# Optimization experiments

Hardware: AMD Instinct MI355X
Metric: run time of the kernel (lower is better)

The kernel has to match this reference:

```python
import jax, jax.numpy as jnp
import numpy as np

DEPTH, DIM, M_DIM, K = 3, 16, 16, 8  # depth, emb_dim, EGNN m_dim default, num_nearest_neighbors
LN_EPS = 1e-5


def _gather(x, idx):
    # x: [B,L,...], idx: [B,L,K] -> [B,L,K,...] (per-batch neighbor gather)
    return jax.vmap(lambda xb, ib: xb[ib])(x, idx)


def _lin(k, fi, fo):
    k1, k2 = jax.random.split(k)
    lim = 1.0 / np.sqrt(fi)
    w = jax.random.uniform(k1, (fi, fo), minval=-lim, maxval=lim, dtype=jnp.float32)
    b = jax.random.uniform(k2, (fo,), minval=-lim, maxval=lim, dtype=jnp.float32)
    return w, b


def _stacked(k, fi, fo):
    ws, bs = zip(*[_lin(kk, fi, fo) for kk in jax.random.split(k, DEPTH)])
    return jnp.stack(ws), jnp.stack(bs)


def setup_inputs() -> dict:
    key = jax.random.key(0)
    ks = jax.random.split(key, 16)
    B, L, num_tokens = 16, 1024, 2
    edge_in = 2 * DIM + 1  # feats_i, feats_j, rel_dist
    inp = {}
    inp['coords'] = jax.random.normal(ks[0], (B, L, 3), dtype=jnp.float32) * 3.0
    inp['residues'] = jax.random.randint(ks[1], (B, L), 0, num_tokens)
    inp['lengths'] = jax.random.randint(ks[2], (B,), L // 2, L + 1)
    inp['token_emb'] = jax.random.normal(ks[3], (num_tokens, DIM), dtype=jnp.float32)
    inp['pos_emb'] = jax.random.normal(ks[4], (L, DIM), dtype=jnp.float32)
    inp['edge_w1'], inp['edge_b1'] = _stacked(ks[5], edge_in, edge_in * 2)
    inp['edge_w2'], inp['edge_b2'] = _stacked(ks[6], edge_in * 2, M_DIM)
    inp['coors_w1'], inp['coors_b1'] = _stacked(ks[7], M_DIM, M_DIM * 4)
    inp['coors_w2'], inp['coors_b2'] = _stacked(ks[8], M_DIM * 4, 1)
    inp['ln_g'] = jnp.ones((DEPTH, DIM), jnp.float32)
    inp['ln_b'] = jnp.zeros((DEPTH, DIM), jnp.float32)
    inp['node_w1'], inp['node_b1'] = _stacked(ks[9], DIM + M_DIM, DIM * 2)
    inp['node_w2'], inp['node_b2'] = _stacked(ks[10], DIM * 2, DIM)
    inp['final_w'], inp['final_b'] = _lin(ks[11], DIM, 3)
    return inp


def reference(coords, residues, lengths, token_emb, pos_emb,
              edge_w1, edge_b1, edge_w2, edge_b2,
              coors_w1, coors_b1, coors_w2, coors_b2,
              ln_g, ln_b, node_w1, node_b1, node_w2, node_b2,
              final_w, final_b):
    B, L, _ = coords.shape
    silu = jax.nn.silu
    mask = jnp.arange(L)[None, :] < lengths[:, None]                 # [B,L]
    pair_mask = mask[:, :, None] & mask[:, None, :]                  # [B,L,L]
    eye = jnp.eye(L, dtype=bool)
    # chain adjacency: i <-> i+1 where both endpoints are within length
    r = jnp.arange(L - 1)
    chain = jnp.zeros((L, L), bool).at[r, r + 1].set(True)
    chain = chain | chain.T
    adj = (chain[None] & pair_mask) & ~eye                           # [B,L,L]

    feats = token_emb[residues] + pos_emb[None, :L]                  # [B,L,D]
    coors = coords
    for d in range(DEPTH):
        # pairwise squared distances for kNN ranking (memory-bound)
        rel_dist_full = jnp.sum((coors[:, :, None] - coors[:, None, :]) ** 2, -1)  # [B,L,L]
        ranking = jnp.where(pair_mask, rel_dist_full, 1e5)
        ranking = jnp.where(eye, -1.0, ranking)   # self always selected first
        ranking = jnp.where(adj, 0.0, ranking)    # adjacency edges forced in
        _, idx = jax.lax.top_k(-ranking, K)                           # [B,L,K] smallest
        mask_j = _gather(mask, idx)
        emask = mask[:, :, None] & mask_j                             # [B,L,K] (valid_radius=inf)
        coors_j = _gather(coors, idx)                                 # [B,L,K,3]
        rel_coors = coors[:, :, None] - coors_j                       # [B,L,K,3]
        rel_dist = jnp.sum(rel_coors ** 2, -1, keepdims=True)         # [B,L,K,1]
        feats_j = _gather(feats, idx)                                 # [B,L,K,D]
        feats_i = jnp.broadcast_to(feats[:, :, None], feats_j.shape)
        edge_in = jnp.concatenate([feats_i, feats_j, rel_dist], -1)   # [B,L,K,2D+1]
        h = silu(edge_in @ edge_w1[d] + edge_b1[d])
        m_ij = silu(h @ edge_w2[d] + edge_b2[d])                      # [B,L,K,M]
        # equivariant coordinate update
        w = silu(m_ij @ coors_w1[d] + coors_b1[d]) @ coors_w2[d] + coors_b2[d]
        w = jnp.where(emask[..., None], w, 0.0)[..., 0]               # [B,L,K]
        coors = coors + jnp.einsum('blk,blkc->blc', w, rel_coors)
        # node update (norm_feats=True in EGNN_Network -> LayerNorm)
        m_i = jnp.sum(jnp.where(emask[..., None], m_ij, 0.0), 2)      # [B,L,M]
        mu = feats.mean(-1, keepdims=True)
        var = jnp.mean((feats - mu) ** 2, -1, keepdims=True)
        normed = (feats - mu) / jnp.sqrt(var + LN_EPS) * ln_g[d] + ln_b[d]
        nin = jnp.concatenate([normed, m_i], -1)                      # [B,L,D+M]
        feats = feats + (silu(nin @ node_w1[d] + node_b1[d]) @ node_w2[d] + node_b2[d])
    delta = feats @ final_w + final_b                                 # [B,L,3]
    return delta
```

## Files before the change

### kernel.cpp

```cpp
#include <hip/hip_runtime.h>
#include <math.h>

typedef unsigned long long u64;
typedef unsigned int u32;

#define NB 16
#define SL 1024
#define DIM 16
#define MDIM 16
#define KNN 8
#define CH 64
#define NHID 32
#define LN_EPS 1e-5f
#define PST 144

__device__ __forceinline__ float silu_f(float x) {
    const float e = __expf(-x);
    return x * __builtin_amdgcn_rcpf(1.0f + e);
}

__global__ __launch_bounds__(256) void init_kernel(
    const float* __restrict__ coords, const int* __restrict__ residues,
    const float* __restrict__ token_emb, const float* __restrict__ pos_emb,
    const float* __restrict__ w1tp, const float* __restrict__ g_eb1,
    float* __restrict__ coordsA, float* __restrict__ featsA,
    float* __restrict__ Pout)
{
    const int t = blockIdx.x * 256 + threadIdx.x;
    const int node = t >> 2;
    const int part = t & 3;
    const int l = node & (SL - 1);
    const int r = residues[node];
    float f[16];
    {
        const float4* te = (const float4*)(token_emb + (size_t)r * DIM);
        const float4* pe = (const float4*)(pos_emb + (size_t)l * DIM);
#pragma unroll
        for (int q = 0; q < 4; ++q) {
            float4 a = te[q], b4 = pe[q];
            f[4*q+0] = a.x + b4.x; f[4*q+1] = a.y + b4.y;
            f[4*q+2] = a.z + b4.z; f[4*q+3] = a.w + b4.w;
        }
    }
    if (part == 0) {
        float4* fo = (float4*)(featsA + (size_t)node * DIM);
#pragma unroll
        for (int q = 0; q < 4; ++q)
            fo[q] = make_float4(f[4*q], f[4*q+1], f[4*q+2], f[4*q+3]);
        coordsA[node * 3 + 0] = coords[node * 3 + 0];
        coordsA[node * 3 + 1] = coords[node * 3 + 1];
        coordsA[node * 3 + 2] = coords[node * 3 + 2];
    }
    const int ubase = (part & 1) * 33;
    const int wbase = (part < 2) ? 0 : 66;
    float res[36];
    res[33] = 0.f; res[34] = 0.f; res[35] = 0.f;
#pragma unroll
    for (int oo = 0; oo < 33; ++oo) {
        const int u = ubase + oo;
        const float* wr = w1tp + (wbase + u) * 16;
        float a0 = (part < 2) ? g_eb1[u] : 0.0f;
        float a1 = 0.f, a2 = 0.f, a3 = 0.f;
#pragma unroll
        for (int c = 0; c < 16; c += 4) {
            a0 = fmaf(f[c + 0], wr[c + 0], a0);
            a1 = fmaf(f[c + 1], wr[c + 1], a1);
            a2 = fmaf(f[c + 2], wr[c + 2], a2);
            a3 = fmaf(f[c + 3], wr[c + 3], a3);
        }
        res[oo] = (a0 + a1) + (a2 + a3);
    }
    float4* op = (float4*)(Pout + (size_t)node * PST + part * 36);
#pragma unroll
    for (int q = 0; q < 9; ++q)
        op[q] = make_float4(res[4*q], res[4*q+1], res[4*q+2], res[4*q+3]);
}

__global__ __launch_bounds__(256) void pack_kernel(
    const float* __restrict__ ew1, const float* __restrict__ ew2,
    const float* __restrict__ cw1,
    const float* __restrict__ nw1, const float* __restrict__ nw2,
    float* __restrict__ w1tp, float* __restrict__ w1rp, float* __restrict__ w2p,
    float* __restrict__ cw1t, float* __restrict__ nw1t, float* __restrict__ nw2t)
{
    const int stride = gridDim.x * 256;
    const int t0 = blockIdx.x * 256 + threadIdx.x;
    for (int idx = t0; idx < 3 * 132 * 16; idx += stride) {
        int d = idx / (132 * 16); int r = idx - d * 132 * 16; int o = r >> 4; int c = r & 15;
        int u = (o < 66) ? o : (o - 66);
        int cc = (o < 66) ? c : (16 + c);
        w1tp[idx] = ew1[(d * 33 + cc) * 66 + u];
    }
    for (int idx = t0; idx < 3 * 72; idx += stride) {
        int d = idx / 72; int o = idx - d * 72; int hh = o / 36; int uu = o - hh * 36;
        w1rp[idx] = (uu < 33) ? ew1[(d * 33 + 32) * 66 + hh * 33 + uu] : 0.0f;
    }
    for (int idx = t0; idx < 3 * 72 * 16; idx += stride) {
        int d = idx / (72 * 16); int r = idx - d * 72 * 16; int u = r >> 4; int v = r & 15;
        int hh = u / 36; int uu = u - hh * 36;
        w2p[idx] = (uu < 33) ? ew2[(d * 66 + hh * 33 + uu) * 16 + v] : 0.0f;
    }
    for (int idx = t0; idx < 3 * CH * 16; idx += stride) {
        int d = idx / (CH * 16); int r = idx - d * CH * 16; int t = r >> 4; int v = r & 15;
        cw1t[(d * CH + t) * 16 + v] = cw1[(d * 16 + v) * CH + t];
    }
    for (int idx = t0; idx < 3 * NHID * 32; idx += stride) {
        int d = idx / (NHID * 32); int r = idx - d * NHID * 32; int u = r >> 5; int c = r & 31;
        nw1t[(d * NHID + u) * 32 + c] = nw1[(d * 32 + c) * NHID + u];
    }
    for (int idx = t0; idx < 3 * 16 * 32; idx += stride) {
        int d = idx / (16 * 32); int r = idx - d * 16 * 32; int c = r >> 5; int u = r & 31;
        nw2t[(d * 16 + c) * 32 + u] = nw2[(d * 32 + u) * 16 + c];
    }
}

__device__ __forceinline__ void merge8(u32* a, const u32* bb) {
    u32 c[8];
#pragma unroll
    for (int t = 0; t < 8; ++t) c[t] = min(a[t], bb[7 - t]);
#define MCAS(x, y) { u32 mn = min(c[x], c[y]); u32 mx = max(c[x], c[y]); c[x] = mn; c[y] = mx; }
    MCAS(0, 4) MCAS(1, 5) MCAS(2, 6) MCAS(3, 7)
    MCAS(0, 2) MCAS(1, 3) MCAS(4, 6) MCAS(5, 7)
    MCAS(0, 1) MCAS(2, 3) MCAS(4, 5) MCAS(6, 7)
#undef MCAS
#pragma unroll
    for (int t = 0; t < 8; ++t) a[t] = c[t];
}

__global__ __launch_bounds__(1024, 8) void knn_kernel(
    const float* __restrict__ coords, const int* __restrict__ lengths,
    int* __restrict__ idxbuf)
{
    __shared__ __align__(16) float4 s_cand[SL];
    __shared__ u32 lists[32][32][9];
    const int tid = threadIdx.x;
    const int b = blockIdx.x >> 5;
    const int i0 = (blockIdx.x & 31) << 5;
    const int len = lengths[b];
    const float* cb = coords + (size_t)b * SL * 3;
    for (int idx = tid; idx < SL; idx += 1024) {
        const float* cp = cb + idx * 3;
        s_cand[idx] = make_float4(cp[0], cp[1], cp[2], 0.0f);
    }
    __syncthreads();

    const int wv = tid >> 6;
    const int lane = tid & 63;
    const int q = lane & 31;
    const int s = (wv << 1) | (lane >> 5);
    const int i = i0 + q;
    const bool mi = i < len;
    const float4 qi = s_cand[i];
    const float xi = qi.x, yi = qi.y, zi = qi.z;

    u32 lst[8];
#pragma unroll
    for (int t = 0; t < 8; ++t) lst[t] = 0xFFFFFFFFu;

    const int jbase = s << 5;
#pragma unroll 4
    for (int jj = 0; jj < 32; ++jj) {
        const int j = jbase + jj;
        const float4 cj = s_cand[j];
        const float dx = xi - cj.x, dy = yi - cj.y, dz = zi - cj.z;
        const float dist = dx * dx + dy * dy + dz * dz;
        const int dij = j - i;
        const bool pm = mi && (j < len);
        const bool adjx = (dij == 1) | (dij == -1);
        float v = pm ? (adjx ? 0.0f : dist) : 1e5f;
        v = (dij == 0) ? -1.0f : v;
        u32 bits = __float_as_uint(v);
        bits ^= (u32)((int)bits >> 31) | 0x80000000u;
        const u32 key = (bits & 0xFFFFFC00u) | (u32)j;
#pragma unroll
        for (int p = 7; p >= 1; --p)
            lst[p] = min(max(key, lst[p - 1]), lst[p]);
        lst[0] = min(key, lst[0]);
    }

#pragma unroll
    for (int t = 0; t < 8; ++t) lists[s][q][t] = lst[t];
    __syncthreads();

    if (tid < 512) {
        const int p = tid >> 5, qq = tid & 31;
        u32 a[8], bb[8];
#pragma unroll
        for (int t = 0; t < 8; ++t) { a[t] = lists[2 * p][qq][t]; bb[t] = lists[2 * p + 1][qq][t]; }
        merge8(a, bb);
#pragma unroll
        for (int t = 0; t < 8; ++t) lists[2 * p][qq][t] = a[t];
    }
    __syncthreads();
    if (tid < 256) {
        const int p = tid >> 5, qq = tid & 31;
        u32 a[8], bb[8];
#pragma unroll
        for (int t = 0; t < 8; ++t) { a[t] = lists[4 * p][qq][t]; bb[t] = lists[4 * p + 2][qq][t]; }
        merge8(a, bb);
#pragma unroll
        for (int t = 0; t < 8; ++t) lists[4 * p][qq][t] = a[t];
    }
    __syncthreads();
    if (tid < 128) {
        const int p = tid >> 5, qq = tid & 31;
        u32 a[8], bb[8];
#pragma unroll
        for (int t = 0; t < 8; ++t) { a[t] = lists[8 * p][qq][t]; bb[t] = lists[8 * p + 4][qq][t]; }
        merge8(a, bb);
#pragma unroll
        for (int t = 0; t < 8; ++t) lists[8 * p][qq][t] = a[t];
    }
    __syncthreads();
    if (tid < 64) {
        const int p = tid >> 5, qq = tid & 31;
        u32 a[8], bb[8];
#pragma unroll
        for (int t = 0; t < 8; ++t) { a[t] = lists[16 * p][qq][t]; bb[t] = lists[16 * p + 8][qq][t]; }
        merge8(a, bb);
#pragma unroll
        for (int t = 0; t < 8; ++t) lists[16 * p][qq][t] = a[t];
    }
    __syncthreads();
    if (tid < 32) {
        const int qq = tid;
        u32 a[8], bb[8];
#pragma unroll
        for (int t = 0; t < 8; ++t) { a[t] = lists[0][qq][t]; bb[t] = lists[16][qq][t]; }
        merge8(a, bb);
        const size_t node = (size_t)b * SL + i0 + qq;
        int4 r0 = make_int4((int)(a[0] & 1023u), (int)(a[1] & 1023u), (int)(a[2] & 1023u), (int)(a[3] & 1023u));
        int4 r1 = make_int4((int)(a[4] & 1023u), (int)(a[5] & 1023u), (int)(a[6] & 1023u), (int)(a[7] & 1023u));
        ((int4*)idxbuf)[node * 2 + 0] = r0;
        ((int4*)idxbuf)[node * 2 + 1] = r1;
    }
}

__global__ __launch_bounds__(256, 3) void layer_kernel(
    const int d,
    const float* __restrict__ coordsIn, float* __restrict__ coordsOut,
    const float* __restrict__ featsIn, float* __restrict__ featsOut,
    const float* __restrict__ Pbuf,
    const int* __restrict__ idxbuf, const int* __restrict__ lengths,
    const float* __restrict__ w1rp, const float* __restrict__ w2p,
    const float* __restrict__ g_eb2,
    const float* __restrict__ cw1t, const float* __restrict__ g_cb1,
    const float* __restrict__ g_cw2, const float* __restrict__ g_cb2,
    const float* __restrict__ g_lng, const float* __restrict__ g_lnb,
    const float* __restrict__ nw1t, const float* __restrict__ g_nb1,
    const float* __restrict__ nw2t, const float* __restrict__ g_nb2,
    const float* __restrict__ w1tp_all, const float* __restrict__ g_eb1,
    float* __restrict__ PbufOut)
{
    __shared__ float s_w2e[72 * 16];
    __shared__ __align__(16) float s_w1r[72];
    __shared__ float s_cw1[CH * 16];
    __shared__ float s_cw2v[CH];
    __shared__ float s_nw1[NHID * 36];
    __shared__ float s_nw2[16 * 36];
    __shared__ float s_eb2[16], s_cb1[CH];
    __shared__ float s_lng[16], s_lnb[16], s_nb1[32], s_nb2[16];
    __shared__ float s_cb2v;

    const int tid = threadIdx.x;
    for (int t = tid; t < 72 * 16; t += 256) s_w2e[t] = w2p[d * 72 * 16 + t];
    for (int t = tid; t < CH * 16; t += 256) s_cw1[t] = cw1t[d * CH * 16 + t];
    for (int t = tid; t < NHID * 32; t += 256) s_nw1[(t >> 5) * 36 + (t & 31)] = nw1t[d * NHID * 32 + t];
    for (int t = tid; t < 16 * 32; t += 256) s_nw2[(t >> 5) * 36 + (t & 31)] = nw2t[d * 16 * 32 + t];
    if (tid < 72) s_w1r[tid] = w1rp[d * 72 + tid];
    if (tid < CH) { s_cw2v[tid] = g_cw2[d * CH + tid]; s_cb1[tid] = g_cb1[d * CH + tid]; }
    if (tid < 16) {
        s_eb2[tid] = g_eb2[d * 16 + tid];
        s_lng[tid] = g_lng[d * 16 + tid];
        s_lnb[tid] = g_lnb[d * 16 + tid];
        s_nb2[tid] = g_nb2[d * 16 + tid];
    }
    if (tid < 32) s_nb1[tid] = g_nb1[d * 32 + tid];
    if (tid == 0) s_cb2v = g_cb2[d];

    const int lane = tid & 63;
    const int h = (lane >> 3) & 1;
    const int k = lane & 7;
    const int sub = lane & 15;
    const int nA = blockIdx.x * 32 + (tid >> 4);
    const int nB = nA + 16;
    const int b = nA >> 10;
    const int len = lengths[b];
    const int jA = idxbuf[nA * 8 + k];
    const int jB = idxbuf[nB * 8 + k];
    const bool emA = ((nA & 1023) < len) && (jA < len);
    const bool emB = ((nB & 1023) < len) && (jB < len);

    float ciA[3], relA[3], ciB[3], relB[3];
    {
        const float* cpA = coordsIn + (size_t)nA * 3;
        const float* cqA = coordsIn + ((size_t)b * SL + jA) * 3;
        ciA[0] = cpA[0]; ciA[1] = cpA[1]; ciA[2] = cpA[2];
        relA[0] = ciA[0] - cqA[0]; relA[1] = ciA[1] - cqA[1]; relA[2] = ciA[2] - cqA[2];
        const float* cpB = coordsIn + (size_t)nB * 3;
        const float* cqB = coordsIn + ((size_t)b * SL + jB) * 3;
        ciB[0] = cpB[0]; ciB[1] = cpB[1]; ciB[2] = cpB[2];
        relB[0] = ciB[0] - cqB[0]; relB[1] = ciB[1] - cqB[1]; relB[2] = ciB[2] - cqB[2];
    }
    const float rdA = fmaf(relA[0], relA[0], fmaf(relA[1], relA[1], relA[2] * relA[2]));
    const float rdB = fmaf(relB[0], relB[0], fmaf(relB[1], relB[1], relB[2] * relB[2]));

    const int ub = h * 36;
    const float* PiA = Pbuf + (size_t)nA * PST + ub;
    const float* PjA = Pbuf + ((size_t)b * SL + jA) * PST + 72 + ub;
    const float* PiB = Pbuf + (size_t)nB * PST + ub;
    const float* PjB = Pbuf + ((size_t)b * SL + jB) * PST + 72 + ub;

    __syncthreads();

    float maccA[16], maccB[16];
#pragma unroll
    for (int v = 0; v < 16; ++v) {
        const float e0 = h ? 0.0f : s_eb2[v];
        maccA[v] = e0; maccB[v] = e0;
    }
#pragma unroll
    for (int c4 = 0; c4 < 9; ++c4) {
        const float4 paA = *(const float4*)(PiA + 4 * c4);
        const float4 pbA = *(const float4*)(PjA + 4 * c4);
        const float4 paB = *(const float4*)(PiB + 4 * c4);
        const float4 pbB = *(const float4*)(PjB + 4 * c4);
        const int u0 = ub + c4 * 4;
        const float4 w1r4 = *(const float4*)&s_w1r[u0];
        const float huA0 = silu_f(fmaf(rdA, w1r4.x, paA.x + pbA.x));
        const float huA1 = silu_f(fmaf(rdA, w1r4.y, paA.y + pbA.y));
        const float huA2 = silu_f(fmaf(rdA, w1r4.z, paA.z + pbA.z));
        const float huA3 = silu_f(fmaf(rdA, w1r4.w, paA.w + pbA.w));
        const float huB0 = silu_f(fmaf(rdB, w1r4.x, paB.x + pbB.x));
        const float huB1 = silu_f(fmaf(rdB, w1r4.y, paB.y + pbB.y));
        const float huB2 = silu_f(fmaf(rdB, w1r4.z, paB.z + pbB.z));
        const float huB3 = silu_f(fmaf(rdB, w1r4.w, paB.w + pbB.w));
        const float* w2r = &s_w2e[u0 * 16];
#pragma unroll
        for (int v = 0; v < 16; ++v) {
            const float w0 = w2r[v], w1 = w2r[16 + v], w2_ = w2r[32 + v], w3 = w2r[48 + v];
            maccA[v] = fmaf(huA3, w3, fmaf(huA2, w2_, fmaf(huA1, w1, fmaf(huA0, w0, maccA[v]))));
            maccB[v] = fmaf(huB3, w3, fmaf(huB2, w2_, fmaf(huB1, w1, fmaf(huB0, w0, maccB[v]))));
        }
    }

#pragma unroll
    for (int v = 0; v < 16; ++v) {
        maccA[v] = silu_f(maccA[v] + __shfl_xor(maccA[v], 8, 64));
        maccB[v] = silu_f(maccB[v] + __shfl_xor(maccB[v], 8, 64));
    }

    const int tb = h * 32;
    float waA = 0.f, waB = 0.f;
#pragma unroll 4
    for (int tt = 0; tt < 32; ++tt) {
        const float* cr = &s_cw1[(tb + tt) * 16];
        const float bias = s_cb1[tb + tt];
        float a0A = bias, a1A = 0.f, a0B = bias, a1B = 0.f;
#pragma unroll
        for (int v = 0; v < 16; v += 2) {
            a0A = fmaf(maccA[v], cr[v], a0A);
            a1A = fmaf(maccA[v + 1], cr[v + 1], a1A);
            a0B = fmaf(maccB[v], cr[v], a0B);
            a1B = fmaf(maccB[v + 1], cr[v + 1], a1B);
        }
        const float cw2v = s_cw2v[tb + tt];
        waA = fmaf(silu_f(a0A + a1A), cw2v, waA);
        waB = fmaf(silu_f(a0B + a1B), cw2v, waB);
    }
    const float waoA = __shfl_xor(waA, 8, 64);
    const float waoB = __shfl_xor(waB, 8, 64);
    const float weA = emA ? (waA + waoA + s_cb2v) : 0.f;
    const float weB = emB ? (waB + waoB + s_cb2v) : 0.f;

    float wr0A = weA * relA[0], wr1A = weA * relA[1], wr2A = weA * relA[2];
    float wr0B = weB * relB[0], wr1B = weB * relB[1], wr2B = weB * relB[2];
#pragma unroll
    for (int s = 1; s < 8; s <<= 1) {
        wr0A += __shfl_xor(wr0A, s, 64);
        wr1A += __shfl_xor(wr1A, s, 64);
        wr2A += __shfl_xor(wr2A, s, 64);
        wr0B += __shfl_xor(wr0B, s, 64);
        wr1B += __shfl_xor(wr1B, s, 64);
        wr2B += __shfl_xor(wr2B, s, 64);
    }
    if ((lane & 15) == 0) {
        coordsOut[(size_t)nA * 3 + 0] = ciA[0] + wr0A;
        coordsOut[(size_t)nA * 3 + 1] = ciA[1] + wr1A;
        coordsOut[(size_t)nA * 3 + 2] = ciA[2] + wr2A;
        coordsOut[(size_t)nB * 3 + 0] = ciB[0] + wr0B;
        coordsOut[(size_t)nB * 3 + 1] = ciB[1] + wr1B;
        coordsOut[(size_t)nB * 3 + 2] = ciB[2] + wr2B;
    }

#pragma unroll
    for (int v = 0; v < 16; ++v) {
        maccA[v] = emA ? maccA[v] : 0.f;
        maccB[v] = emB ? maccB[v] : 0.f;
#pragma unroll
        for (int s = 1; s < 8; s <<= 1) {
            maccA[v] += __shfl_xor(maccA[v], s, 64);
            maccB[v] += __shfl_xor(maccB[v], s, 64);
        }
    }

    float fiA[16], fiB[16];
    {
        const float4* ppA = (const float4*)(featsIn + (size_t)nA * DIM);
        float4 a0 = ppA[0], a1 = ppA[1], a2 = ppA[2], a3 = ppA[3];
        fiA[0]=a0.x; fiA[1]=a0.y; fiA[2]=a0.z; fiA[3]=a0.w;
        fiA[4]=a1.x; fiA[5]=a1.y; fiA[6]=a1.z; fiA[7]=a1.w;
        fiA[8]=a2.x; fiA[9]=a2.y; fiA[10]=a2.z; fiA[11]=a2.w;
        fiA[12]=a3.x; fiA[13]=a3.y; fiA[14]=a3.z; fiA[15]=a3.w;
        const float4* ppB = (const float4*)(featsIn + (size_t)nB * DIM);
        float4 b0 = ppB[0], b1 = ppB[1], b2 = ppB[2], b3 = ppB[3];
        fiB[0]=b0.x; fiB[1]=b0.y; fiB[2]=b0.z; fiB[3]=b0.w;
        fiB[4]=b1.x; fiB[5]=b1.y; fiB[6]=b1.z; fiB[7]=b1.w;
        fiB[8]=b2.x; fiB[9]=b2.y; fiB[10]=b2.z; fiB[11]=b2.w;
        fiB[12]=b3.x; fiB[13]=b3.y; fiB[14]=b3.z; fiB[15]=b3.w;
    }
    const float fiSubA = featsIn[(size_t)nA * DIM + sub];
    const float fiSubB = featsIn[(size_t)nB * DIM + sub];

    {
        float mu = 0.f;
#pragma unroll
        for (int c = 0; c < 16; ++c) mu += fiA[c];
        mu *= 0.0625f;
        float var = 0.f;
#pragma unroll
        for (int c = 0; c < 16; ++c) { const float dd = fiA[c] - mu; var = fmaf(dd, dd, var); }
        var *= 0.0625f;
        const float rs = rsqrtf(var + LN_EPS);
#pragma unroll
        for (int c = 0; c < 16; ++c) fiA[c] = fmaf((fiA[c] - mu) * rs, s_lng[c], s_lnb[c]);
    }
    {
        float mu = 0.f;
#pragma unroll
        for (int c = 0; c < 16; ++c) mu += fiB[c];
        mu *= 0.0625f;
        float var = 0.f;
#pragma unroll
        for (int c = 0; c < 16; ++c) { const float dd = fiB[c] - mu; var = fmaf(dd, dd, var); }
        var *= 0.0625f;
        const float rs = rsqrtf(var + LN_EPS);
#pragma unroll
        for (int c = 0; c < 16; ++c) fiB[c] = fmaf((fiB[c] - mu) * rs, s_lng[c], s_lnb[c]);
    }

    float nhA[2], nhB[2];
#pragma unroll
    for (int q = 0; q < 2; ++q) {
        const int u = sub * 2 + q;
        const float* nr = &s_nw1[u * 36];
        const float bias = s_nb1[u];
        float a0A = bias, a1A = 0.f, a0B = bias, a1B = 0.f;
#pragma unroll
        for (int c = 0; c < 16; c += 2) {
            a0A = fmaf(fiA[c], nr[c], a0A);
            a1A = fmaf(fiA[c + 1], nr[c + 1], a1A);
            a0B = fmaf(fiB[c], nr[c], a0B);
            a1B = fmaf(fiB[c + 1], nr[c + 1], a1B);
        }
#pragma unroll
        for (int v = 0; v < 16; v += 2) {
            a0A = fmaf(maccA[v], nr[16 + v], a0A);
            a1A = fmaf(maccA[v + 1], nr[16 + v + 1], a1A);
            a0B = fmaf(maccB[v], nr[16 + v], a0B);
            a1B = fmaf(maccB[v + 1], nr[16 + v + 1], a1B);
        }
        nhA[q] = silu_f(a0A + a1A);
        nhB[q] = silu_f(a0B + a1B);
    }

    const int nbase = lane & ~15;
    const float* w2c = &s_nw2[sub * 36];
    float oA = s_nb2[sub], oB = s_nb2[sub];
#pragma unroll
    for (int u = 0; u < 32; ++u) {
        const float w = w2c[u];
        oA = fmaf(__shfl(nhA[u & 1], nbase + (u >> 1), 64), w, oA);
        oB = fmaf(__shfl(nhB[u & 1], nbase + (u >> 1), 64), w, oB);
    }
    const float foA = fiSubA + oA;
    const float foB = fiSubB + oB;
    featsOut[(size_t)nA * DIM + sub] = foA;
    featsOut[(size_t)nB * DIM + sub] = foB;

    if (d < 2) {
        float frA[16], frB[16];
#pragma unroll
        for (int c = 0; c < 16; ++c) {
            frA[c] = __shfl(foA, nbase + c, 64);
            frB[c] = __shfl(foB, nbase + c, 64);
        }
        const float* wbase = w1tp_all + (d + 1) * 132 * 16;
        const float* bbase = g_eb1 + (d + 1) * 66;
        float* PoutA = PbufOut + (size_t)nA * PST;
        float* PoutB = PbufOut + (size_t)nB * PST;
#pragma unroll
        for (int q = 0; q < 9; ++q) {
            const int col = sub + (q << 4);
            const int ch = (col >= 108) ? 3 : (col >= 72) ? 2 : (col >= 36) ? 1 : 0;
            const int uu = col - ch * 36;
            const bool valid = uu < 33;
            const int u = ((ch & 1) ? 33 : 0) + uu;
            const int uc = valid ? u : 0;
            const int widx = valid ? ((ch < 2) ? u : 66 + u) : 0;
            const float bias = (valid && ch < 2) ? bbase[uc] : 0.0f;
            float a0A = bias, a1A = 0.f, a2A = 0.f, a3A = 0.f;
            float a0B = bias, a1B = 0.f, a2B = 0.f, a3B = 0.f;
            const float* wr = wbase + widx * 16;
#pragma unroll
            for (int cc = 0; cc < 16; cc += 4) {
                const float w0 = wr[cc + 0], w1 = wr[cc + 1], w2_ = wr[cc + 2], w3 = wr[cc + 3];
                a0A = fmaf(frA[cc + 0], w0, a0A);
                a1A = fmaf(frA[cc + 1], w1, a1A);
                a2A = fmaf(frA[cc + 2], w2_, a2A);
                a3A = fmaf(frA[cc + 3], w3, a3A);
                a0B = fmaf(frB[cc + 0], w0, a0B);
                a1B = fmaf(frB[cc + 1], w1, a1B);
                a2B = fmaf(frB[cc + 2], w2_, a2B);
                a3B = fmaf(frB[cc + 3], w3, a3B);
            }
            PoutA[col] = valid ? ((a0A + a1A) + (a2A + a3A)) : 0.0f;
            PoutB[col] = valid ? ((a0B + a1B) + (a2B + a3B)) : 0.0f;
        }
    }
}

__global__ __launch_bounds__(256) void final_kernel(
    const float* __restrict__ feats, const float* __restrict__ fw,
    const float* __restrict__ fb, float* __restrict__ out)
{
    const int nid = blockIdx.x * 256 + threadIdx.x;
    if (nid >= NB * SL) return;
    float f[DIM];
#pragma unroll
    for (int c = 0; c < DIM; ++c) f[c] = feats[nid * DIM + c];
#pragma unroll
    for (int o = 0; o < 3; ++o) {
        float acc = fb[o];
#pragma unroll
        for (int c = 0; c < DIM; ++c) acc = fmaf(f[c], fw[c * 3 + o], acc);
        out[nid * 3 + o] = acc;
    }
}

extern "C" void kernel_launch(void* const* d_in, const int* in_sizes, int n_in,
                              void* d_out, int out_size, void* d_ws, size_t ws_size,
                              hipStream_t stream) {
    const float* coords    = (const float*)d_in[0];
    const int*   residues  = (const int*)d_in[1];
    const int*   lengths   = (const int*)d_in[2];
    const float* token_emb = (const float*)d_in[3];
    const float* pos_emb   = (const float*)d_in[4];
    const float* ew1 = (const float*)d_in[5];
    const float* eb1 = (const float*)d_in[6];
    const float* ew2 = (const float*)d_in[7];
    const float* eb2 = (const float*)d_in[8];
    const float* cw1 = (const float*)d_in[9];
    const float* cb1 = (const float*)d_in[10];
    const float* cw2 = (const float*)d_in[11];
    const float* cb2 = (const float*)d_in[12];
    const float* lng = (const float*)d_in[13];
    const float* lnb = (const float*)d_in[14];
    const float* nw1 = (const float*)d_in[15];
    const float* nb1 = (const float*)d_in[16];
    const float* nw2 = (const float*)d_in[17];
    const float* nb2 = (const float*)d_in[18];
    const float* fw  = (const float*)d_in[19];
    const float* fb  = (const float*)d_in[20];

    float* ws = (float*)d_ws;
    float* coordsA = ws;
    float* coordsB = coordsA + NB * SL * 3;
    float* featsA  = coordsB + NB * SL * 3;
    float* featsB  = featsA + NB * SL * DIM;
    int*   idxbuf  = (int*)(featsB + NB * SL * DIM);
    float* w1tp = (float*)(idxbuf + NB * SL * KNN);
    float* w1rp = w1tp + 3 * 132 * 16;
    float* w2p  = w1rp + 3 * 72;
    float* cw1t = w2p + 3 * 72 * 16;
    float* nw1t = cw1t + 3 * CH * 16;
    float* nw2t = nw1t + 3 * NHID * 32;
    float* PbufA = nw2t + 3 * 16 * 32;
    float* PbufB = PbufA + (size_t)NB * SL * PST;

    pack_kernel<<<32, 256, 0, stream>>>(ew1, ew2, cw1, nw1, nw2, w1tp, w1rp, w2p, cw1t, nw1t, nw2t);
    init_kernel<<<NB * SL * 4 / 256, 256, 0, stream>>>(coords, residues, token_emb, pos_emb,
                                                        w1tp, eb1, coordsA, featsA, PbufA);

    float* cIn = coordsA; float* cOut = coordsB;
    float* fIn = featsA;  float* fOut = featsB;
    float* pIn = PbufA;   float* pOut = PbufB;
    for (int d = 0; d < 3; ++d) {
        knn_kernel<<<NB * SL / 32, 1024, 0, stream>>>(cIn, lengths, idxbuf);
        layer_kernel<<<NB * SL * KNN / 256, 256, 0, stream>>>(d, cIn, cOut, fIn, fOut, pIn, idxbuf, lengths,
            w1rp, w2p, eb2, cw1t, cb1, cw2, cb2, lng, lnb, nw1t, nb1, nw2t, nb2,
            w1tp, eb1, pOut);
        float* t;
        t = cIn; cIn = cOut; cOut = t;
        t = fIn; fIn = fOut; fOut = t;
        t = pIn; pIn = pOut; pOut = t;
    }

    final_kernel<<<NB * SL / 256, 256, 0, stream>>>(fIn, fw, fb, (float*)d_out);
}
```

Before: 273.4 us.

## Fuse KNN search, layer update and final projection into one kernel per layer

Merges the separate KNN kernel and per-layer message-passing kernel into a single kernel whose blocks first compute neighbour lists for their 32 nodes and then process those same nodes, reusing one shared-memory buffer. The final linear projection is folded into the last layer's iteration, removing a launch. KNN now uses 256 threads per block with 128 candidates per thread, which reduces parallelism in the search phase and lowers occupancy hints.

```diff
diff --git a/kernel.cpp b/kernel.cpp
--- a/kernel.cpp
+++ b/kernel.cpp
@@ -7,7 +7,6 @@
 #define NB 16
 #define SL 1024
 #define DIM 16
-#define MDIM 16
 #define KNN 8
 #define CH 64
 #define NHID 32
@@ -127,121 +126,12 @@
     for (int t = 0; t < 8; ++t) a[t] = c[t];
 }
 
-__global__ __launch_bounds__(1024, 8) void knn_kernel(
-    const float* __restrict__ coords, const int* __restrict__ lengths,
-    int* __restrict__ idxbuf)
-{
-    __shared__ __align__(16) float4 s_cand[SL];
-    __shared__ u32 lists[32][32][9];
-    const int tid = threadIdx.x;
-    const int b = blockIdx.x >> 5;
-    const int i0 = (blockIdx.x & 31) << 5;
-    const int len = lengths[b];
-    const float* cb = coords + (size_t)b * SL * 3;
-    for (int idx = tid; idx < SL; idx += 1024) {
-        const float* cp = cb + idx * 3;
-        s_cand[idx] = make_float4(cp[0], cp[1], cp[2], 0.0f);
-    }
-    __syncthreads();
-
-    const int wv = tid >> 6;
-    const int lane = tid & 63;
-    const int q = lane & 31;
-    const int s = (wv << 1) | (lane >> 5);
-    const int i = i0 + q;
-    const bool mi = i < len;
-    const float4 qi = s_cand[i];
-    const float xi = qi.x, yi = qi.y, zi = qi.z;
-
-    u32 lst[8];
-#pragma unroll
-    for (int t = 0; t < 8; ++t) lst[t] = 0xFFFFFFFFu;
-
-    const int jbase = s << 5;
-#pragma unroll 4
-    for (int jj = 0; jj < 32; ++jj) {
-        const int j = jbase + jj;
-        const float4 cj = s_cand[j];
-        const float dx = xi - cj.x, dy = yi - cj.y, dz = zi - cj.z;
-        const float dist = dx * dx + dy * dy + dz * dz;
-        const int dij = j - i;
-        const bool pm = mi && (j < len);
-        const bool adjx = (dij == 1) | (dij == -1);
-        float v = pm ? (adjx ? 0.0f : dist) : 1e5f;
-        v = (dij == 0) ? -1.0f : v;
-        u32 bits = __float_as_uint(v);
-        bits ^= (u32)((int)bits >> 31) | 0x80000000u;
-        const u32 key = (bits & 0xFFFFFC00u) | (u32)j;
-#pragma unroll
-        for (int p = 7; p >= 1; --p)
-            lst[p] = min(max(key, lst[p - 1]), lst[p]);
-        lst[0] = min(key, lst[0]);
-    }
-
-#pragma unroll
-    for (int t = 0; t < 8; ++t) lists[s][q][t] = lst[t];
-    __syncthreads();
-
-    if (tid < 512) {
-        const int p = tid >> 5, qq = tid & 31;
-        u32 a[8], bb[8];
-#pragma unroll
-        for (int t = 0; t < 8; ++t) { a[t] = lists[2 * p][qq][t]; bb[t] = lists[2 * p + 1][qq][t]; }
-        merge8(a, bb);
-#pragma unroll
-        for (int t = 0; t < 8; ++t) lists[2 * p][qq][t] = a[t];
-    }
-    __syncthreads();
-    if (tid < 256) {
-        const int p = tid >> 5, qq = tid & 31;
-        u32 a[8], bb[8];
-#pragma unroll
-        for (int t = 0; t < 8; ++t) { a[t] = lists[4 * p][qq][t]; bb[t] = lists[4 * p + 2][qq][t]; }
-        merge8(a, bb);
-#pragma unroll
-        for (int t = 0; t < 8; ++t) lists[4 * p][qq][t] = a[t];
-    }
-    __syncthreads();
-    if (tid < 128) {
-        const int p = tid >> 5, qq = tid & 31;
-        u32 a[8], bb[8];
-#pragma unroll
-        for (int t = 0; t < 8; ++t) { a[t] = lists[8 * p][qq][t]; bb[t] = lists[8 * p + 4][qq][t]; }
-        merge8(a, bb);
-#pragma unroll
-        for (int t = 0; t < 8; ++t) lists[8 * p][qq][t] = a[t];
-    }
-    __syncthreads();
-    if (tid < 64) {
-        const int p = tid >> 5, qq = tid & 31;
-        u32 a[8], bb[8];
-#pragma unroll
-        for (int t = 0; t < 8; ++t) { a[t] = lists[16 * p][qq][t]; bb[t] = lists[16 * p + 8][qq][t]; }
-        merge8(a, bb);
-#pragma unroll
-        for (int t = 0; t < 8; ++t) lists[16 * p][qq][t] = a[t];
-    }
-    __syncthreads();
-    if (tid < 32) {
-        const int qq = tid;
-        u32 a[8], bb[8];
-#pragma unroll
-        for (int t = 0; t < 8; ++t) { a[t] = lists[0][qq][t]; bb[t] = lists[16][qq][t]; }
-        merge8(a, bb);
-        const size_t node = (size_t)b * SL + i0 + qq;
-        int4 r0 = make_int4((int)(a[0] & 1023u), (int)(a[1] & 1023u), (int)(a[2] & 1023u), (int)(a[3] & 1023u));
-        int4 r1 = make_int4((int)(a[4] & 1023u), (int)(a[5] & 1023u), (int)(a[6] & 1023u), (int)(a[7] & 1023u));
-        ((int4*)idxbuf)[node * 2 + 0] = r0;
-        ((int4*)idxbuf)[node * 2 + 1] = r1;
-    }
-}
-
-__global__ __launch_bounds__(256, 3) void layer_kernel(
+__global__ __launch_bounds__(256, 2) void fused_kernel(
     const int d,
     const float* __restrict__ coordsIn, float* __restrict__ coordsOut,
     const float* __restrict__ featsIn, float* __restrict__ featsOut,
-    const float* __restrict__ Pbuf,
-    const int* __restrict__ idxbuf, const int* __restrict__ lengths,
+    const float* __restrict__ Pbuf, float* __restrict__ PbufOut,
+    int* __restrict__ idxbuf, const int* __restrict__ lengths,
     const float* __restrict__ w1rp, const float* __restrict__ w2p,
     const float* __restrict__ g_eb2,
     const float* __restrict__ cw1t, const float* __restrict__ g_cb1,
@@ -250,301 +140,396 @@
     const float* __restrict__ nw1t, const float* __restrict__ g_nb1,
     const float* __restrict__ nw2t, const float* __restrict__ g_nb2,
     const float* __restrict__ w1tp_all, const float* __restrict__ g_eb1,
-    float* __restrict__ PbufOut)
+    const float* __restrict__ fw, const float* __restrict__ fb,
+    float* __restrict__ gout)
 {
-    __shared__ float s_w2e[72 * 16];
-    __shared__ __align__(16) float s_w1r[72];
-    __shared__ float s_cw1[CH * 16];
-    __shared__ float s_cw2v[CH];
-    __shared__ float s_nw1[NHID * 36];
-    __shared__ float s_nw2[16 * 36];
-    __shared__ float s_eb2[16], s_cb1[CH];
-    __shared__ float s_lng[16], s_lnb[16], s_nb1[32], s_nb2[16];
-    __shared__ float s_cb2v;
-
+    __shared__ __align__(16) char smem[25600];
     const int tid = threadIdx.x;
-    for (int t = tid; t < 72 * 16; t += 256) s_w2e[t] = w2p[d * 72 * 16 + t];
-    for (int t = tid; t < CH * 16; t += 256) s_cw1[t] = cw1t[d * CH * 16 + t];
-    for (int t = tid; t < NHID * 32; t += 256) s_nw1[(t >> 5) * 36 + (t & 31)] = nw1t[d * NHID * 32 + t];
-    for (int t = tid; t < 16 * 32; t += 256) s_nw2[(t >> 5) * 36 + (t & 31)] = nw2t[d * 16 * 32 + t];
-    if (tid < 72) s_w1r[tid] = w1rp[d * 72 + tid];
-    if (tid < CH) { s_cw2v[tid] = g_cw2[d * CH + tid]; s_cb1[tid] = g_cb1[d * CH + tid]; }
-    if (tid < 16) {
-        s_eb2[tid] = g_eb2[d * 16 + tid];
-        s_lng[tid] = g_lng[d * 16 + tid];
-        s_lnb[tid] = g_lnb[d * 16 + tid];
-        s_nb2[tid] = g_nb2[d * 16 + tid];
-    }
-    if (tid < 32) s_nb1[tid] = g_nb1[d * 32 + tid];
-    if (tid == 0) s_cb2v = g_cb2[d];
-
     const int lane = tid & 63;
-    const int h = (lane >> 3) & 1;
-    const int k = lane & 7;
-    const int sub = lane & 15;
-    const int nA = blockIdx.x * 32 + (tid >> 4);
-    const int nB = nA + 16;
-    const int b = nA >> 10;
-    const int len = lengths[b];
-    const int jA = idxbuf[nA * 8 + k];
-    const int jB = idxbuf[nB * 8 + k];
-    const bool emA = ((nA & 1023) < len) && (jA < len);
-    const bool emB = ((nB & 1023) < len) && (jB < len);
-
-    float ciA[3], relA[3], ciB[3], relB[3];
+
     {
-        const float* cpA = coordsIn + (size_t)nA * 3;
-        const float* cqA = coordsIn + ((size_t)b * SL + jA) * 3;
-        ciA[0] = cpA[0]; ciA[1] = cpA[1]; ciA[2] = cpA[2];
-        relA[0] = ciA[0] - cqA[0]; relA[1] = ciA[1] - cqA[1]; relA[2] = ciA[2] - cqA[2];
-        const float* cpB = coordsIn + (size_t)nB * 3;
-        const float* cqB = coordsIn + ((size_t)b * SL + jB) * 3;
-        ciB[0] = cpB[0]; ciB[1] = cpB[1]; ciB[2] = cpB[2];
-        relB[0] = ciB[0] - cqB[0]; relB[1] = ciB[1] - cqB[1]; relB[2] = ciB[2] - cqB[2];
-    }
-    const float rdA = fmaf(relA[0], relA[0], fmaf(relA[1], relA[1], relA[2] * relA[2]));
-    const float rdB = fmaf(relB[0], relB[0], fmaf(relB[1], relB[1], relB[2] * relB[2]));
-
-    const int ub = h * 36;
-    const float* PiA = Pbuf + (size_t)nA * PST + ub;
-    const float* PjA = Pbuf + ((size_t)b * SL + jA) * PST + 72 + ub;
-    const float* PiB = Pbuf + (size_t)nB * PST + ub;
-    const float* PjB = Pbuf + ((size_t)b * SL + jB) * PST + 72 + ub;
-
+        float4* s_cand = (float4*)smem;
+        u32* lst_base  = (u32*)(smem + 16384);
+        const int bk = blockIdx.x >> 5;
+        const int i0 = (blockIdx.x & 31) << 5;
+        const int len = lengths[bk];
+        const float* cb = coordsIn + (size_t)bk * SL * 3;
+        for (int idx = tid; idx < SL; idx += 256) {
+            const float* cp = cb + idx * 3;
+            s_cand[idx] = make_float4(cp[0], cp[1], cp[2], 0.0f);
+        }
+        __syncthreads();
+
+        const int q = tid & 31;
+        const int s = tid >> 5;
+        const int i = i0 + q;
+        const bool mi = i < len;
+        const float4 qi = s_cand[i];
+        const float xi = qi.x, yi = qi.y, zi = qi.z;
+
+        u32 lst[8];
+#pragma unroll
+        for (int t = 0; t < 8; ++t) lst[t] = 0xFFFFFFFFu;
+
+        const int jbase = s << 7;
+#pragma unroll 4
+        for (int jj = 0; jj < 128; ++jj) {
+            const int j = jbase + jj;
+            const float4 cj = s_cand[j];
+            const float dx = xi - cj.x, dy = yi - cj.y, dz = zi - cj.z;
+            const float dist = dx * dx + dy * dy + dz * dz;
+            const int dij = j - i;
+            const bool pm = mi && (j < len);
+            const bool adjx = (dij == 1) | (dij == -1);
+            float v = pm ? (adjx ? 0.0f : dist) : 1e5f;
+            v = (dij == 0) ? -1.0f : v;
+            u32 bits = __float_as_uint(v);
+            bits ^= (u32)((int)bits >> 31) | 0x80000000u;
+            const u32 key = (bits & 0xFFFFFC00u) | (u32)j;
+#pragma unroll
+            for (int p = 7; p >= 1; --p)
+                lst[p] = min(max(key, lst[p - 1]), lst[p]);
+            lst[0] = min(key, lst[0]);
+        }
+#pragma unroll
+        for (int t = 0; t < 8; ++t) lst_base[(s * 32 + q) * 9 + t] = lst[t];
+        __syncthreads();
+
+        if (tid < 128) {
+            const int p = tid >> 5, qq = tid & 31;
+            u32 a[8], bb[8];
+#pragma unroll
+            for (int t = 0; t < 8; ++t) {
+                a[t]  = lst_base[((2 * p) * 32 + qq) * 9 + t];
+                bb[t] = lst_base[((2 * p + 1) * 32 + qq) * 9 + t];
+            }
+            merge8(a, bb);
+#pragma unroll
+            for (int t = 0; t < 8; ++t) lst_base[((2 * p) * 32 + qq) * 9 + t] = a[t];
+        }
+        __syncthreads();
+        if (tid < 64) {
+            const int p = tid >> 5, qq = tid & 31;
+            u32 a[8], bb[8];
+#pragma unroll
+            for (int t = 0; t < 8; ++t) {
+                a[t]  = lst_base[((4 * p) * 32 + qq) * 9 + t];
+                bb[t] = lst_base[((4 * p + 2) * 32 + qq) * 9 + t];
+            }
+            merge8(a, bb);
+#pragma unroll
+            for (int t = 0; t < 8; ++t) lst_base[((4 * p) * 32 + qq) * 9 + t] = a[t];
+        }
+        __syncthreads();
+        if (tid < 32) {
+            const int qq = tid;
+            u32 a[8], bb[8];
+#pragma unroll
+            for (int t = 0; t < 8; ++t) {
+                a[t]  = lst_base[(0 * 32 + qq) * 9 + t];
+                bb[t] = lst_base[(4 * 32 + qq) * 9 + t];
+            }
+            merge8(a, bb);
+            const size_t node = (size_t)bk * SL + i0 + qq;
+            int4 r0 = make_int4((int)(a[0] & 1023u), (int)(a[1] & 1023u), (int)(a[2] & 1023u), (int)(a[3] & 1023u));
+            int4 r1 = make_int4((int)(a[4] & 1023u), (int)(a[5] & 1023u), (int)(a[6] & 1023u), (int)(a[7] & 1023u));
+            ((int4*)idxbuf)[node * 2 + 0] = r0;
+            ((int4*)idxbuf)[node * 2 + 1] = r1;
+        }
+    }
     __syncthreads();
 
-    float maccA[16], maccB[16];
-#pragma unroll
-    for (int v = 0; v < 16; ++v) {
-        const float e0 = h ? 0.0f : s_eb2[v];
-        maccA[v] = e0; maccB[v] = e0;
-    }
-#pragma unroll
-    for (int c4 = 0; c4 < 9; ++c4) {
-        const float4 paA = *(const float4*)(PiA + 4 * c4);
-        const float4 pbA = *(const float4*)(PjA + 4 * c4);
-        const float4 paB = *(const float4*)(PiB + 4 * c4);
-        const float4 pbB = *(const float4*)(PjB + 4 * c4);
-        const int u0 = ub + c4 * 4;
-        const float4 w1r4 = *(const float4*)&s_w1r[u0];
-        const float huA0 = silu_f(fmaf(rdA, w1r4.x, paA.x + pbA.x));
-        const float huA1 = silu_f(fmaf(rdA, w1r4.y, paA.y + pbA.y));
-        const float huA2 = silu_f(fmaf(rdA, w1r4.z, paA.z + pbA.z));
-        const float huA3 = silu_f(fmaf(rdA, w1r4.w, paA.w + pbA.w));
-        const float huB0 = silu_f(fmaf(rdB, w1r4.x, paB.x + pbB.x));
-        const float huB1 = silu_f(fmaf(rdB, w1r4.y, paB.y + pbB.y));
-        const float huB2 = silu_f(fmaf(rdB, w1r4.z, paB.z + pbB.z));
-        const float huB3 = silu_f(fmaf(rdB, w1r4.w, paB.w + pbB.w));
-        const float* w2r = &s_w2e[u0 * 16];
+    {
+        float* s_w2e  = (float*)(smem);
+        float* s_cw1  = (float*)(smem + 4608);
+        float* s_nw1  = (float*)(smem + 8704);
+        float* s_nw2  = (float*)(smem + 13312);
+        float* s_w1r  = (float*)(smem + 15616);
+        float* s_cw2v = (float*)(smem + 15904);
+        float* s_cb1  = (float*)(smem + 16160);
+        float* s_eb2  = (float*)(smem + 16416);
+        float* s_lng  = (float*)(smem + 16480);
+        float* s_lnb  = (float*)(smem + 16544);
+        float* s_nb1  = (float*)(smem + 16608);
+        float* s_nb2  = (float*)(smem + 16736);
+        float* s_cb2  = (float*)(smem + 16800);
+
+        for (int t = tid; t < 72 * 16; t += 256) s_w2e[t] = w2p[d * 72 * 16 + t];
+        for (int t = tid; t < CH * 16; t += 256) s_cw1[t] = cw1t[d * CH * 16 + t];
+        for (int t = tid; t < NHID * 32; t += 256) s_nw1[(t >> 5) * 36 + (t & 31)] = nw1t[d * NHID * 32 + t];
+        for (int t = tid; t < 16 * 32; t += 256) s_nw2[(t >> 5) * 36 + (t & 31)] = nw2t[d * 16 * 32 + t];
+        if (tid < 72) s_w1r[tid] = w1rp[d * 72 + tid];
+        if (tid < CH) { s_cw2v[tid] = g_cw2[d * CH + tid]; s_cb1[tid] = g_cb1[d * CH + tid]; }
+        if (tid < 16) {
+            s_eb2[tid] = g_eb2[d * 16 + tid];
+            s_lng[tid] = g_lng[d * 16 + tid];
+            s_lnb[tid] = g_lnb[d * 16 + tid];
+            s_nb2[tid] = g_nb2[d * 16 + tid];
+        }
+        if (tid < 32) s_nb1[tid] = g_nb1[d * 32 + tid];
+        if (tid == 0) s_cb2[0] = g_cb2[d];
+
+        const int h = (lane >> 3) & 1;
+        const int k = lane & 7;
+        const int sub = lane & 15;
+        const int nA = blockIdx.x * 32 + (tid >> 4);
+        const int nB = nA + 16;
+        const int b = nA >> 10;
+        const int len = lengths[b];
+        const int jA = idxbuf[nA * 8 + k];
+        const int jB = idxbuf[nB * 8 + k];
+        const bool emA = ((nA & 1023) < len) && (jA < len);
+        const bool emB = ((nB & 1023) < len) && (jB < len);
+
+        float ciA[3], relA[3], ciB[3], relB[3];
+        {
+            const float* cpA = coordsIn + (size_t)nA * 3;
+            const float* cqA = coordsIn + ((size_t)b * SL + jA) * 3;
+            ciA[0] = cpA[0]; ciA[1] = cpA[1]; ciA[2] = cpA[2];
+            relA[0] = ciA[0] - cqA[0]; relA[1] = ciA[1] - cqA[1]; relA[2] = ciA[2] - cqA[2];
+            const float* cpB = coordsIn + (size_t)nB * 3;
+            const float* cqB = coordsIn + ((size_t)b * SL + jB) * 3;
+            ciB[0] = cpB[0]; ciB[1] = cpB[1]; ciB[2] = cpB[2];
+            relB[0] = ciB[0] - cqB[0]; relB[1] = ciB[1] - cqB[1]; relB[2] = ciB[2] - cqB[2];
+        }
+        const float rdA = fmaf(relA[0], relA[0], fmaf(relA[1], relA[1], relA[2] * relA[2]));
+        const float rdB = fmaf(relB[0], relB[0], fmaf(relB[1], relB[1], relB[2] * relB[2]));
+
+        const int ub = h * 36;
+        const float* PiA = Pbuf + (size_t)nA * PST + ub;
+        const float* PjA = Pbuf + ((size_t)b * SL + jA) * PST + 72 + ub;
+        const float* PiB = Pbuf + (size_t)nB * PST + ub;
+        const float* PjB = Pbuf + ((size_t)b * SL + jB) * PST + 72 + ub;
+
+        __syncthreads();
+
+        float maccA[16], maccB[16];
 #pragma unroll
         for (int v = 0; v < 16; ++v) {
-            const float w0 = w2r[v], w1 = w2r[16 + v], w2_ = w2r[32 + v], w3 = w2r[48 + v];
-            maccA[v] = fmaf(huA3, w3, fmaf(huA2, w2_, fmaf(huA1, w1, fmaf(huA0, w0, maccA[v]))));
-            maccB[v] = fmaf(huB3, w3, fmaf(huB2, w2_, fmaf(huB1, w1, fmaf(huB0, w0, maccB[v]))));
-        }
-    }
-
-#pragma unroll
-    for (int v = 0; v < 16; ++v) {
-        maccA[v] = silu_f(maccA[v] + __shfl_xor(maccA[v], 8, 64));
-        maccB[v] = silu_f(maccB[v] + __shfl_xor(maccB[v], 8, 64));
-    }
-
-    const int tb = h * 32;
-    float waA = 0.f, waB = 0.f;
+            const float e0 = h ? 0.0f : s_eb2[v];
+            maccA[v] = e0; maccB[v] = e0;
+        }
+#pragma unroll
+        for (int c4 = 0; c4 < 9; ++c4) {
+            const float4 paA = *(const float4*)(PiA + 4 * c4);
+            const float4 pbA = *(const float4*)(PjA + 4 * c4);
+            const float4 paB = *(const float4*)(PiB + 4 * c4);
+            const float4 pbB = *(const float4*)(PjB + 4 * c4);
+            const int u0 = ub + c4 * 4;
+            const float4 w1r4 = *(const float4*)&s_w1r[u0];
+            const float huA0 = silu_f(fmaf(rdA, w1r4.x, paA.x + pbA.x));
+            const float huA1 = silu_f(fmaf(rdA, w1r4.y, paA.y + pbA.y));
+            const float huA2 = silu_f(fmaf(rdA, w1r4.z, paA.z + pbA.z));
+            const float huA3 = silu_f(fmaf(rdA, w1r4.w, paA.w + pbA.w));
+            const float huB0 = silu_f(fmaf(rdB, w1r4.x, paB.x + pbB.x));
+            const float huB1 = silu_f(fmaf(rdB, w1r4.y, paB.y + pbB.y));
+            const float huB2 = silu_f(fmaf(rdB, w1r4.z, paB.z + pbB.z));
+            const float huB3 = silu_f(fmaf(rdB, w1r4.w, paB.w + pbB.w));
+            const float* w2r = &s_w2e[u0 * 16];
+#pragma unroll
+            for (int v = 0; v < 16; ++v) {
+                const float w0 = w2r[v], w1 = w2r[16 + v], w2_ = w2r[32 + v], w3 = w2r[48 + v];
+                maccA[v] = fmaf(huA3, w3, fmaf(huA2, w2_, fmaf(huA1, w1, fmaf(huA0, w0, maccA[v]))));
+                maccB[v] = fmaf(huB3, w3, fmaf(huB2, w2_, fmaf(huB1, w1, fmaf(huB0, w0, maccB[v]))));
+            }
+        }
+
+#pragma unroll
+        for (int v = 0; v < 16; ++v) {
+            maccA[v] = silu_f(maccA[v] + __shfl_xor(maccA[v], 8, 64));
+            maccB[v] = silu_f(maccB[v] + __shfl_xor(maccB[v], 8, 64));
+        }
+
+        const int tb = h * 32;
+        float waA = 0.f, waB = 0.f;
 #pragma unroll 4
-    for (int tt = 0; tt < 32; ++tt) {
-        const float* cr = &s_cw1[(tb + tt) * 16];
-        const float bias = s_cb1[tb + tt];
-        float a0A = bias, a1A = 0.f, a0B = bias, a1B = 0.f;
-#pragma unroll
-        for (int v = 0; v < 16; v += 2) {
-            a0A = fmaf(maccA[v], cr[v], a0A);
-            a1A = fmaf(maccA[v + 1], cr[v + 1], a1A);
-            a0B = fmaf(maccB[v], cr[v], a0B);
-            a1B = fmaf(maccB[v + 1], cr[v + 1], a1B);
-        }
-        const float cw2v = s_cw2v[tb + tt];
-        waA = fmaf(silu_f(a0A + a1A), cw2v, waA);
-        waB = fmaf(silu_f(a0B + a1B), cw2v, waB);
-    }
-    const float waoA = __shfl_xor(waA, 8, 64);
-    const float waoB = __shfl_xor(waB, 8, 64);
-    const float weA = emA ? (waA + waoA + s_cb2v) : 0.f;
-    const float weB = emB ? (waB + waoB + s_cb2v) : 0.f;
-
-    float wr0A = weA * relA[0], wr1A = weA * relA[1], wr2A = weA * relA[2];
-    float wr0B = weB * relB[0], wr1B = weB * relB[1], wr2B = weB * relB[2];
-#pragma unroll
-    for (int s = 1; s < 8; s <<= 1) {
-        wr0A += __shfl_xor(wr0A, s, 64);
-        wr1A += __shfl_xor(wr1A, s, 64);
-        wr2A += __shfl_xor(wr2A, s, 64);
-        wr0B += __shfl_xor(wr0B, s, 64);
-        wr1B += __shfl_xor(wr1B, s, 64);
-        wr2B += __shfl_xor(wr2B, s, 64);
-    }
-    if ((lane & 15) == 0) {
-        coordsOut[(size_t)nA * 3 + 0] = ciA[0] + wr0A;
-        coordsOut[(size_t)nA * 3 + 1] = ciA[1] + wr1A;
-        coordsOut[(size_t)nA * 3 + 2] = ciA[2] + wr2A;
-        coordsOut[(size_t)nB * 3 + 0] = ciB[0] + wr0B;
-        coordsOut[(size_t)nB * 3 + 1] = ciB[1] + wr1B;
-        coordsOut[(size_t)nB * 3 + 2] = ciB[2] + wr2B;
-    }
-
-#pragma unroll
-    for (int v = 0; v < 16; ++v) {
-        maccA[v] = emA ? maccA[v] : 0.f;
-        maccB[v] = emB ? maccB[v] : 0.f;
+        for (int tt = 0; tt < 32; ++tt) {
+            const float* cr = &s_cw1[(tb + tt) * 16];
+            const float bias = s_cb1[tb + tt];
+            float a0A = bias, a1A = 0.f, a0B = bias, a1B = 0.f;
+#pragma unroll
+            for (int v = 0; v < 16; v += 2) {
+                a0A = fmaf(maccA[v], cr[v], a0A);
+                a1A = fmaf(maccA[v + 1], cr[v + 1], a1A);
+                a0B = fmaf(maccB[v], cr[v], a0B);
+                a1B = fmaf(maccB[v + 1], cr[v + 1], a1B);
+            }
+            const float cw2v = s_cw2v[tb + tt];
+            waA = fmaf(silu_f(a0A + a1A), cw2v, waA);
+            waB = fmaf(silu_f(a0B + a1B), cw2v, waB);
+        }
+        const float waoA = __shfl_xor(waA, 8, 64);
+        const float waoB = __shfl_xor(waB, 8, 64);
+        const float weA = emA ? (waA + waoA + s_cb2[0]) : 0.f;
+        const float weB = emB ? (waB + waoB + s_cb2[0]) : 0.f;
+
+        float wr0A = weA * relA[0], wr1A = weA * relA[1], wr2A = weA * relA[2];
+        float wr0B = weB * relB[0], wr1B = weB * relB[1], wr2B = weB * relB[2];
 #pragma unroll
         for (int s = 1; s < 8; s <<= 1) {
-            maccA[v] += __shfl_xor(maccA[v], s, 64);
-            maccB[v] += __shfl_xor(maccB[v], s, 64);
-        }
-    }
-
-    float fiA[16], fiB[16];
-    {
-        const float4* ppA = (const float4*)(featsIn + (size_t)nA * DIM);
-        float4 a0 = ppA[0], a1 = ppA[1], a2 = ppA[2], a3 = ppA[3];
-        fiA[0]=a0.x; fiA[1]=a0.y; fiA[2]=a0.z; fiA[3]=a0.w;
-        fiA[4]=a1.x; fiA[5]=a1.y; fiA[6]=a1.z; fiA[7]=a1.w;
-        fiA[8]=a2.x; fiA[9]=a2.y; fiA[10]=a2.z; fiA[11]=a2.w;
-        fiA[12]=a3.x; fiA[13]=a3.y; fiA[14]=a3.z; fiA[15]=a3.w;
-        const float4* ppB = (const float4*)(featsIn + (size_t)nB * DIM);
-        float4 b0 = ppB[0], b1 = ppB[1], b2 = ppB[2], b3 = ppB[3];
-        fiB[0]=b0.x; fiB[1]=b0.y; fiB[2]=b0.z; fiB[3]=b0.w;
-        fiB[4]=b1.x; fiB[5]=b1.y; fiB[6]=b1.z; fiB[7]=b1.w;
-        fiB[8]=b2.x; fiB[9]=b2.y; fiB[10]=b2.z; fiB[11]=b2.w;
-        fiB[12]=b3.x; fiB[13]=b3.y; fiB[14]=b3.z; fiB[15]=b3.w;
-    }
-    const float fiSubA = featsIn[(size_t)nA * DIM + sub];
-    const float fiSubB = featsIn[(size_t)nB * DIM + sub];
-
-    {
-        float mu = 0.f;
-#pragma unroll
-        for (int c = 0; c < 16; ++c) mu += fiA[c];
-        mu *= 0.0625f;
-        float var = 0.f;
-#pragma unroll
-        for (int c = 0; c < 16; ++c) { const float dd = fiA[c] - mu; var = fmaf(dd, dd, var); }
-        var *= 0.0625f;
-        const float rs = rsqrtf(var + LN_EPS);
-#pragma unroll
-        for (int c = 0; c < 16; ++c) fiA[c] = fmaf((fiA[c] - mu) * rs, s_lng[c], s_lnb[c]);
-    }
-    {
-        float mu = 0.f;
-#pragma unroll
-        for (int c = 0; c < 16; ++c) mu += fiB[c];
-        mu *= 0.0625f;
-        float var = 0.f;
-#pragma unroll
-        for (int c = 0; c < 16; ++c) { const float dd = fiB[c] - mu; var = fmaf(dd, dd, var); }
-        var *= 0.0625f;
-        const float rs = rsqrtf(var + LN_EPS);
-#pragma unroll
-        for (int c = 0; c < 16; ++c) fiB[c] = fmaf((fiB[c] - mu) * rs, s_lng[c], s_lnb[c]);
-    }
-
-    float nhA[2], nhB[2];
-#pragma unroll
-    for (int q = 0; q < 2; ++q) {
-        const int u = sub * 2 + q;
-        const float* nr = &s_nw1[u * 36];
-        const float bias = s_nb1[u];
-        float a0A = bias, a1A = 0.f, a0B = bias, a1B = 0.f;
-#pragma unroll
-        for (int c = 0; c < 16; c += 2) {
-            a0A = fmaf(fiA[c], nr[c], a0A);
-            a1A = fmaf(fiA[c + 1], nr[c + 1], a1A);
-            a0B = fmaf(fiB[c], nr[c], a0B);
-            a1B = fmaf(fiB[c + 1], nr[c + 1], a1B);
-        }
-#pragma unroll
-        for (int v = 0; v < 16; v += 2) {
-            a0A = fmaf(maccA[v], nr[16 + v], a0A);
-            a1A = fmaf(maccA[v + 1], nr[16 + v + 1], a1A);
-            a0B = fmaf(maccB[v], nr[16 + v], a0B);
-            a1B = fmaf(maccB[v + 1], nr[16 + v + 1], a1B);
-        }
-        nhA[q] = silu_f(a0A + a1A);
-        nhB[q] = silu_f(a0B + a1B);
-    }
-
-    const int nbase = lane & ~15;
-    const float* w2c = &s_nw2[sub * 36];
-    float oA = s_nb2[sub], oB = s_nb2[sub];
-#pragma unroll
-    for (int u = 0; u < 32; ++u) {
-        const float w = w2c[u];
-        oA = fmaf(__shfl(nhA[u & 1], nbase + (u >> 1), 64), w, oA);
-        oB = fmaf(__shfl(nhB[u & 1], nbase + (u >> 1), 64), w, oB);
-    }
-    const float foA = fiSubA + oA;
-    const float foB = fiSubB + oB;
-    featsOut[(size_t)nA * DIM + sub] = foA;
-    featsOut[(size_t)nB * DIM + sub] = foB;
-
-    if (d < 2) {
+            wr0A += __shfl_xor(wr0A, s, 64);
+            wr1A += __shfl_xor(wr1A, s, 64);
+            wr2A += __shfl_xor(wr2A, s, 64);
+            wr0B += __shfl_xor(wr0B, s, 64);
+            wr1B += __shfl_xor(wr1B, s, 64);
+            wr2B += __shfl_xor(wr2B, s, 64);
+        }
+        if ((lane & 15) == 0) {
+            coordsOut[(size_t)nA * 3 + 0] = ciA[0] + wr0A;
+            coordsOut[(size_t)nA * 3 + 1] = ciA[1] + wr1A;
+            coordsOut[(size_t)nA * 3 + 2] = ciA[2] + wr2A;
+            coordsOut[(size_t)nB * 3 + 0] = ciB[0] + wr0B;
+            coordsOut[(size_t)nB * 3 + 1] = ciB[1] + wr1B;
+            coordsOut[(size_t)nB * 3 + 2] = ciB[2] + wr2B;
+        }
+
+#pragma unroll
+        for (int v = 0; v < 16; ++v) {
+            maccA[v] = emA ? maccA[v] : 0.f;
+            maccB[v] = emB ? maccB[v] : 0.f;
+#pragma unroll
+            for (int s = 1; s < 8; s <<= 1) {
+                maccA[v] += __shfl_xor(maccA[v], s, 64);
+                maccB[v] += __shfl_xor(maccB[v], s, 64);
+            }
+        }
+
+        float fiA[16], fiB[16];
+        {
+            const float4* ppA = (const float4*)(featsIn + (size_t)nA * DIM);
+            float4 a0 = ppA[0], a1 = ppA[1], a2 = ppA[2], a3 = ppA[3];
+            fiA[0]=a0.x; fiA[1]=a0.y; fiA[2]=a0.z; fiA[3]=a0.w;
+            fiA[4]=a1.x; fiA[5]=a1.y; fiA[6]=a1.z; fiA[7]=a1.w;
+            fiA[8]=a2.x; fiA[9]=a2.y; fiA[10]=a2.z; fiA[11]=a2.w;
+            fiA[12]=a3.x; fiA[13]=a3.y; fiA[14]=a3.z; fiA[15]=a3.w;
+            const float4* ppB = (const float4*)(featsIn + (size_t)nB * DIM);
+            float4 b0 = ppB[0], b1 = ppB[1], b2 = ppB[2], b3 = ppB[3];
+            fiB[0]=b0.x; fiB[1]=b0.y; fiB[2]=b0.z; fiB[3]=b0.w;
+            fiB[4]=b1.x; fiB[5]=b1.y; fiB[6]=b1.z; fiB[7]=b1.w;
+            fiB[8]=b2.x; fiB[9]=b2.y; fiB[10]=b2.z; fiB[11]=b2.w;
+            fiB[12]=b3.x; fiB[13]=b3.y; fiB[14]=b3.z; fiB[15]=b3.w;
+        }
+        const float fiSubA = featsIn[(size_t)nA * DIM + sub];
+        const float fiSubB = featsIn[(size_t)nB * DIM + sub];
+
+        {
+            float mu = 0.f;
+#pragma unroll
+            for (int c = 0; c < 16; ++c) mu += fiA[c];
+            mu *= 0.0625f;
+            float var = 0.f;
+#pragma unroll
+            for (int c = 0; c < 16; ++c) { const float dd = fiA[c] - mu; var = fmaf(dd, dd, var); }
+            var *= 0.0625f;
+            const float rs = rsqrtf(var + LN_EPS);
+#pragma unroll
+            for (int c = 0; c < 16; ++c) fiA[c] = fmaf((fiA[c] - mu) * rs, s_lng[c], s_lnb[c]);
+        }
+        {
+            float mu = 0.f;
+#pragma unroll
+            for (int c = 0; c < 16; ++c) mu += fiB[c];
+            mu *= 0.0625f;
+            float var = 0.f;
+#pragma unroll
+            for (int c = 0; c < 16; ++c) { const float dd = fiB[c] - mu; var = fmaf(dd, dd, var); }
+            var *= 0.0625f;
+            const float rs = rsqrtf(var + LN_EPS);
+#pragma unroll
+            for (int c = 0; c < 16; ++c) fiB[c] = fmaf((fiB[c] - mu) * rs, s_lng[c], s_lnb[c]);
+        }
+
+        float nhA[2], nhB[2];
+#pragma unroll
+        for (int q2 = 0; q2 < 2; ++q2) {
+            const int u = sub * 2 + q2;
+            const float* nr = &s_nw1[u * 36];
+            const float bias = s_nb1[u];
+            float a0A = bias, a1A = 0.f, a0B = bias, a1B = 0.f;
+#pragma unroll
+            for (int c = 0; c < 16; c += 2) {
+                a0A = fmaf(fiA[c], nr[c], a0A);
+                a1A = fmaf(fiA[c + 1], nr[c + 1], a1A);
+                a0B = fmaf(fiB[c], nr[c], a0B);
+                a1B = fmaf(fiB[c + 1], nr[c + 1], a1B);
+            }
+#pragma unroll
+            for (int v = 0; v < 16; v += 2) {
+                a0A = fmaf(maccA[v], nr[16 + v], a0A);
+                a1A = fmaf(maccA[v + 1], nr[16 + v + 1], a1A);
+                a0B = fmaf(maccB[v], nr[16 + v], a0B);
+                a1B = fmaf(maccB[v + 1], nr[16 + v + 1], a1B);
+            }
+            nhA[q2] = silu_f(a0A + a1A);
+            nhB[q2] = silu_f(a0B + a1B);
+        }
+
+        const int nbase = lane & ~15;
+        const float* w2c = &s_nw2[sub * 36];
+        float oA = s_nb2[sub], oB = s_nb2[sub];
+#pragma unroll
+        for (int u = 0; u < 32; ++u) {
+            const float w = w2c[u];
+            oA = fmaf(__shfl(nhA[u & 1], nbase + (u >> 1), 64), w, oA);
+            oB = fmaf(__shfl(nhB[u & 1], nbase + (u >> 1), 64), w, oB);
+        }
+        const float foA = fiSubA + oA;
+        const float foB = fiSubB + oB;
+        featsOut[(size_t)nA * DIM + sub] = foA;
+        featsOut[(size_t)nB * DIM + sub] = foB;
+
         float frA[16], frB[16];
 #pragma unroll
         for (int c = 0; c < 16; ++c) {
             frA[c] = __shfl(foA, nbase + c, 64);
             frB[c] = __shfl(foB, nbase + c, 64);
         }
-        const float* wbase = w1tp_all + (d + 1) * 132 * 16;
-        const float* bbase = g_eb1 + (d + 1) * 66;
-        float* PoutA = PbufOut + (size_t)nA * PST;
-        float* PoutB = PbufOut + (size_t)nB * PST;
-#pragma unroll
-        for (int q = 0; q < 9; ++q) {
-            const int col = sub + (q << 4);
-            const int ch = (col >= 108) ? 3 : (col >= 72) ? 2 : (col >= 36) ? 1 : 0;
-            const int uu = col - ch * 36;
-            const bool valid = uu < 33;
-            const int u = ((ch & 1) ? 33 : 0) + uu;
-            const int uc = valid ? u : 0;
-            const int widx = valid ? ((ch < 2) ? u : 66 + u) : 0;
-            const float bias = (valid && ch < 2) ? bbase[uc] : 0.0f;
-            float a0A = bias, a1A = 0.f, a2A = 0.f, a3A = 0.f;
-            float a0B = bias, a1B = 0.f, a2B = 0.f, a3B = 0.f;
-            const float* wr = wbase + widx * 16;
-#pragma unroll
-            for (int cc = 0; cc < 16; cc += 4) {
-                const float w0 = wr[cc + 0], w1 = wr[cc + 1], w2_ = wr[cc + 2], w3 = wr[cc + 3];
-                a0A = fmaf(frA[cc + 0], w0, a0A);
-                a1A = fmaf(frA[cc + 1], w1, a1A);
-                a2A = fmaf(frA[cc + 2], w2_, a2A);
-                a3A = fmaf(frA[cc + 3], w3, a3A);
-                a0B = fmaf(frB[cc + 0], w0, a0B);
-                a1B = fmaf(frB[cc + 1], w1, a1B);
-                a2B = fmaf(frB[cc + 2], w2_, a2B);
-                a3B = fmaf(frB[cc + 3], w3, a3B);
-            }
-            PoutA[col] = valid ? ((a0A + a1A) + (a2A + a3A)) : 0.0f;
-            PoutB[col] = valid ? ((a0B + a1B) + (a2B + a3B)) : 0.0f;
-        }
-    }
-}
-
-__global__ __launch_bounds__(256) void final_kernel(
-    const float* __restrict__ feats, const float* __restrict__ fw,
-    const float* __restrict__ fb, float* __restrict__ out)
-{
-    const int nid = blockIdx.x * 256 + threadIdx.x;
-    if (nid >= NB * SL) return;
-    float f[DIM];
-#pragma unroll
-    for (int c = 0; c < DIM; ++c) f[c] = feats[nid * DIM + c];
-#pragma unroll
-    for (int o = 0; o < 3; ++o) {
-        float acc = fb[o];
-#pragma unroll
-        for (int c = 0; c < DIM; ++c) acc = fmaf(f[c], fw[c * 3 + o], acc);
-        out[nid * 3 + o] = acc;
+
+        if (d < 2) {
+            const float* wbase = w1tp_all + (d + 1) * 132 * 16;
+            const float* bbase = g_eb1 + (d + 1) * 66;
+            float* PoutA = PbufOut + (size_t)nA * PST;
+            float* PoutB = PbufOut + (size_t)nB * PST;
+#pragma unroll
+            for (int q2 = 0; q2 < 9; ++q2) {
+                const int col = sub + (q2 << 4);
+                const int ch = (col >= 108) ? 3 : (col >= 72) ? 2 : (col >= 36) ? 1 : 0;
+                const int uu = col - ch * 36;
+                const bool valid = uu < 33;
+                const int u = ((ch & 1) ? 33 : 0) + uu;
+                const int uc = valid ? u : 0;
+                const int widx = valid ? ((ch < 2) ? u : 66 + u) : 0;
+                const float bias = (valid && ch < 2) ? bbase[uc] : 0.0f;
+                float a0A = bias, a1A = 0.f, a2A = 0.f, a3A = 0.f;
+                float a0B = bias, a1B = 0.f, a2B = 0.f, a3B = 0.f;
+                const float* wr = wbase + widx * 16;
+#pragma unroll
+                for (int cc = 0; cc < 16; cc += 4) {
+                    const float w0 = wr[cc + 0], w1 = wr[cc + 1], w2_ = wr[cc + 2], w3 = wr[cc + 3];
+                    a0A = fmaf(frA[cc + 0], w0, a0A);
+                    a1A = fmaf(frA[cc + 1], w1, a1A);
+                    a2A = fmaf(frA[cc + 2], w2_, a2A);
+                    a3A = fmaf(frA[cc + 3], w3, a3A);
+                    a0B = fmaf(frB[cc + 0], w0, a0B);
+                    a1B = fmaf(frB[cc + 1], w1, a1B);
+                    a2B = fmaf(frB[cc + 2], w2_, a2B);
+                    a3B = fmaf(frB[cc + 3], w3, a3B);
+                }
+                PoutA[col] = valid ? ((a0A + a1A) + (a2A + a3A)) : 0.0f;
+                PoutB[col] = valid ? ((a0B + a1B) + (a2B + a3B)) : 0.0f;
+            }
+        } else {
+            if (sub < 3) {
+                float accA = fb[sub], accB = fb[sub];
+#pragma unroll
+                for (int c = 0; c < 16; ++c) {
+                    accA = fmaf(frA[c], fw[c * 3 + sub], accA);
+                    accB = fmaf(frB[c], fw[c * 3 + sub], accB);
+                }
+                gout[(size_t)nA * 3 + sub] = accA;
+                gout[(size_t)nB * 3 + sub] = accB;
+            }
+        }
     }
 }
 
@@ -587,6 +572,7 @@
     float* nw2t = nw1t + 3 * NHID * 32;
     float* PbufA = nw2t + 3 * 16 * 32;
     float* PbufB = PbufA + (size_t)NB * SL * PST;
+    float* gout  = (float*)d_out;
 
     pack_kernel<<<32, 256, 0, stream>>>(ew1, ew2, cw1, nw1, nw2, w1tp, w1rp, w2p, cw1t, nw1t, nw2t);
     init_kernel<<<NB * SL * 4 / 256, 256, 0, stream>>>(coords, residues, token_emb, pos_emb,
@@ -596,15 +582,13 @@
     float* fIn = featsA;  float* fOut = featsB;
     float* pIn = PbufA;   float* pOut = PbufB;
     for (int d = 0; d < 3; ++d) {
-        knn_kernel<<<NB * SL / 32, 1024, 0, stream>>>(cIn, lengths, idxbuf);
-        layer_kernel<<<NB * SL * KNN / 256, 256, 0, stream>>>(d, cIn, cOut, fIn, fOut, pIn, idxbuf, lengths,
+        fused_kernel<<<NB * SL / 32, 256, 0, stream>>>(d, cIn, cOut, fIn, fOut, pIn, pOut,
+            idxbuf, lengths,
             w1rp, w2p, eb2, cw1t, cb1, cw2, cb2, lng, lnb, nw1t, nb1, nw2t, nb2,
-            w1tp, eb1, pOut);
+            w1tp, eb1, fw, fb, gout);
         float* t;
         t = cIn; cIn = cOut; cOut = t;
         t = fIn; fIn = fOut; fOut = t;
         t = pIn; pIn = pOut; pOut = t;
     }
-
-    final_kernel<<<NB * SL / 256, 256, 0, stream>>>(fIn, fw, fb, (float*)d_out);
 }
```

New measurement: 256.2 us. 6.3% less time.
